# Kernel optimization log

Measured on AMD Instinct MI355X. Metric: run time of the kernel, lower is better.

The kernel has to match this reference:

```python
import jax, jax.numpy as jnp
import numpy as np

D_IN = 1024
D_OUT = 1024


def setup_inputs() -> dict:
    key = jax.random.key(0)
    kx, kq, kk, kv = jax.random.split(key, 4)
    B, S = 4, 2048
    scale = 1.0 / np.sqrt(D_IN)
    return {
        "x": jax.random.normal(kx, (B, S, D_IN), dtype=jnp.float32),
        "Wq": jax.random.normal(kq, (D_IN, D_OUT), dtype=jnp.float32) * scale,
        "Wk": jax.random.normal(kk, (D_IN, D_OUT), dtype=jnp.float32) * scale,
        "Wv": jax.random.normal(kv, (D_IN, D_OUT), dtype=jnp.float32) * scale,
    }


def reference(x, Wq, Wk, Wv):
    # x: [B, S, D_in]; single-head causal attention (dropout=0 -> identity)
    q = jnp.einsum("bsd,de->bse", x, Wq)
    k = jnp.einsum("bsd,de->bse", x, Wk)
    v = jnp.einsum("bsd,de->bse", x, Wv)
    S = x.shape[1]
    d_k = k.shape[-1]
    scores = jnp.einsum("bqe,bke->bqk", q, k) / jnp.sqrt(jnp.float32(d_k))
    causal = jnp.tril(jnp.ones((S, S), dtype=bool))  # True = keep
    scores = jnp.where(causal, scores, -jnp.inf)
    weights = jax.nn.softmax(scores, axis=-1)
    return jnp.einsum("bqk,bke->bqe", weights, v)
```

## Files before the change

kernel.cpp:

```cpp
#include <hip/hip_runtime.h>

typedef unsigned short u16;
typedef __bf16 bf16x8_v __attribute__((ext_vector_type(8)));
typedef float f32x4 __attribute__((ext_vector_type(4)));

__device__ __forceinline__ u16 f2bf(float f) {
    unsigned u = __float_as_uint(f);
    unsigned r = u + 0x7fffu + ((u >> 16) & 1u);
    return (u16)(r >> 16);
}
__device__ __forceinline__ float bf2f(u16 h) {
    return __uint_as_float(((unsigned)h) << 16);
}

__device__ __forceinline__ void gll16(const u16* g, u16* l) {
    __builtin_amdgcn_global_load_lds(
        (const __attribute__((address_space(1))) void*)g,
        (__attribute__((address_space(3))) void*)l, 16, 0, 0);
}

#define EXP_SHIFT 12.0f

__global__ __launch_bounds__(256) void k_cvt_x(const float* __restrict__ x,
                                               u16* __restrict__ y, int n) {
    int i = (blockIdx.x * 256 + threadIdx.x) * 8;
    if (i < n) {
        float4 a = *(const float4*)(x + i);
        float4 b = *(const float4*)(x + i + 4);
        union { int4 p; u16 h[8]; } o;
        o.h[0] = f2bf(a.x); o.h[1] = f2bf(a.y); o.h[2] = f2bf(a.z); o.h[3] = f2bf(a.w);
        o.h[4] = f2bf(b.x); o.h[5] = f2bf(b.y); o.h[6] = f2bf(b.z); o.h[7] = f2bf(b.w);
        *(int4*)(y + i) = o.p;
    }
}

__global__ __launch_bounds__(256) void k_cvt_w3(const float* __restrict__ Wq,
                                                const float* __restrict__ Wk,
                                                const float* __restrict__ Wv,
                                                u16* __restrict__ Wt3) {
    __shared__ float tile[32][33];
    const int z = blockIdx.z;
    const float* W = (z == 0) ? Wq : (z == 1) ? Wk : Wv;
    u16* Wt = Wt3 + (size_t)z * 1024 * 1024;
    int bx = blockIdx.x;
    int by = blockIdx.y;
    int tx = threadIdx.x & 31;
    int ty = threadIdx.x >> 5;
#pragma unroll
    for (int r = 0; r < 4; ++r)
        tile[ty + r * 8][tx] = W[(by * 32 + ty + r * 8) * 1024 + bx * 32 + tx];
    __syncthreads();
#pragma unroll
    for (int r = 0; r < 4; ++r)
        Wt[(bx * 32 + ty + r * 8) * 1024 + by * 32 + tx] =
            f2bf(tile[tx][ty + r * 8]);
}

__device__ __forceinline__ void gemm_core_nt(const u16* __restrict__ A,
                                             const u16* __restrict__ B,
                                             int lda, int ldb, int kLen,
                                             u16* smem, f32x4 acc[4][4]) {
    u16* As = smem;
    u16* Bs = smem + 128 * 32;
    const int tid = threadIdx.x;
    const int wave = tid >> 6;
    const int lane = tid & 63;
    const int r0 = tid >> 2, o0 = (tid & 3) * 8;
    const int r1 = r0 + 64;
    u16* AsW0 = As + wave * 512;
    u16* AsW1 = As + 2048 + wave * 512;
    u16* BsW0 = Bs + wave * 512;
    u16* BsW1 = Bs + 2048 + wave * 512;

    const int wm = (wave >> 1) * 64;
    const int wn = (wave & 1) * 64;
    const int row16 = lane & 15;
    const int quad = lane >> 4;

#pragma unroll
    for (int i = 0; i < 4; ++i)
#pragma unroll
        for (int j = 0; j < 4; ++j) {
            f32x4 z = {0.f, 0.f, 0.f, 0.f};
            acc[i][j] = z;
        }

    const u16* Ag0 = A + r0 * lda + o0;
    const u16* Ag1 = A + r1 * lda + o0;
    const u16* Bg0 = B + r0 * ldb + o0;
    const u16* Bg1 = B + r1 * ldb + o0;

    const int ktiles = kLen >> 5;
    for (int kt = 0; kt < ktiles; ++kt) {
        __syncthreads();
        gll16(Ag0 + kt * 32, AsW0);
        gll16(Ag1 + kt * 32, AsW1);
        gll16(Bg0 + kt * 32, BsW0);
        gll16(Bg1 + kt * 32, BsW1);
        __syncthreads();
        bf16x8_v af[4], bfv[4];
#pragma unroll
        for (int i = 0; i < 4; ++i)
            af[i] = *(const bf16x8_v*)(As + (wm + i * 16 + row16) * 32 + quad * 8);
#pragma unroll
        for (int j = 0; j < 4; ++j)
            bfv[j] = *(const bf16x8_v*)(Bs + (wn + j * 16 + row16) * 32 + quad * 8);
#pragma unroll
        for (int i = 0; i < 4; ++i)
#pragma unroll
            for (int j = 0; j < 4; ++j)
                acc[i][j] = __builtin_amdgcn_mfma_f32_16x16x32_bf16(
                    af[i], bfv[j], acc[i][j], 0, 0, 0);
    }
}

__device__ __forceinline__ void epi_bf16(const f32x4 acc[4][4], u16* smem,
                                         u16* __restrict__ g, int ldg) {
    const int tid = threadIdx.x;
    const int wave = tid >> 6, lane = tid & 63;
    const int row16 = lane & 15, quad = lane >> 4;
    u16* Ts = smem + wave * 2048;
#pragma unroll
    for (int jh = 0; jh < 2; ++jh) {
#pragma unroll
        for (int i = 0; i < 4; ++i)
#pragma unroll
            for (int jj = 0; jj < 2; ++jj) {
                const int j = jh * 2 + jj;
#pragma unroll
                for (int r = 0; r < 4; ++r)
                    Ts[(i * 16 + quad * 4 + r) * 32 + jj * 16 + row16] =
                        f2bf(acc[i][j][r]);
            }
#pragma unroll
        for (int s = 0; s < 4; ++s) {
            const int row = s * 16 + (lane >> 2);
            int4 val = *(const int4*)(Ts + row * 32 + (lane & 3) * 8);
            *(int4*)(g + (size_t)row * ldg + jh * 32 + (lane & 3) * 8) = val;
        }
    }
}

__global__ __launch_bounds__(256, 3) void k_gemm_proj(const u16* __restrict__ X,
                                                      const u16* __restrict__ Wt3,
                                                      u16* __restrict__ Qb,
                                                      u16* __restrict__ Kb,
                                                      u16* __restrict__ Vt) {
    __shared__ u16 smem[128 * 64];
    const int n0g = blockIdx.x * 128, m0 = blockIdx.y * 128;
    f32x4 acc[4][4];
    gemm_core_nt(X + (size_t)m0 * 1024, Wt3 + (size_t)n0g * 1024, 1024, 1024, 1024,
                 smem, acc);
    const int tid = threadIdx.x, wave = tid >> 6, lane = tid & 63;
    const int wm = (wave >> 1) * 64, wn = (wave & 1) * 64;
    const int row16 = lane & 15, quad = lane >> 4;
    if (n0g < 2048) {
        u16* Y = (n0g < 1024) ? Qb : Kb;
        const int n0 = n0g & 1023;
        __syncthreads();
        epi_bf16(acc, smem, Y + (size_t)(m0 + wm) * 1024 + n0 + wn, 1024);
    } else {
        const int n0 = n0g - 2048;
#pragma unroll
        for (int i = 0; i < 4; ++i)
#pragma unroll
            for (int j = 0; j < 4; ++j) {
                int m = m0 + wm + i * 16 + quad * 4;
                int n = n0 + wn + j * 16 + row16;
                int b = m >> 11, s = m & 2047;
                union { ushort4 u4; u16 h[4]; } o;
#pragma unroll
                for (int r = 0; r < 4; ++r) o.h[r] = f2bf(acc[i][j][r]);
                *(ushort4*)(Vt + ((size_t)b * 1024 + n) * 2048 + s) = o.u4;
            }
    }
}

__global__ __launch_bounds__(256, 3) void k_gemm_scores(const u16* __restrict__ Q,
                                                        const u16* __restrict__ Kb,
                                                        u16* __restrict__ Sb,
                                                        float* __restrict__ Srow) {
    __shared__ u16 smem[128 * 64];
    int t = blockIdx.x, b = blockIdx.y;
    int mt = 0;
    while ((mt + 1) * (mt + 2) / 2 <= t) ++mt;
    int nt = t - mt * (mt + 1) / 2;
    const u16* Qp = Q + (size_t)b * 2048 * 1024 + (size_t)mt * 128 * 1024;
    const u16* Kp = Kb + (size_t)b * 2048 * 1024 + (size_t)nt * 128 * 1024;
    u16* Sp = Sb + (size_t)b * 2048 * 2048;
    f32x4 acc[4][4];
    gemm_core_nt(Qp, Kp, 1024, 1024, 1024, smem, acc);
    const int tid = threadIdx.x, wave = tid >> 6, lane = tid & 63;
    const int wm = (wave >> 1) * 64, wn = (wave & 1) * 64;
    const int row16 = lane & 15, quad = lane >> 4;
    const int mBase = mt * 128 + wm;
    const int nBase = nt * 128 + wn;
    u16* Ts = smem + wave * 2048;
    float rs[4][4];
#pragma unroll
    for (int i = 0; i < 4; ++i)
#pragma unroll
        for (int r = 0; r < 4; ++r) rs[i][r] = 0.f;

    __syncthreads();
#pragma unroll
    for (int jh = 0; jh < 2; ++jh) {
#pragma unroll
        for (int i = 0; i < 4; ++i)
#pragma unroll
            for (int jj = 0; jj < 2; ++jj) {
                const int j = jh * 2 + jj;
                const int n = nBase + jh * 32 + jj * 16 + row16;
#pragma unroll
                for (int r = 0; r < 4; ++r) {
                    const int m = mBase + i * 16 + quad * 4 + r;
                    float e = 0.f;
                    if (n <= m)
                        e = __expf(acc[i][j][r] * 0.03125f - EXP_SHIFT);
                    rs[i][r] += e;
                    Ts[(i * 16 + quad * 4 + r) * 32 + jj * 16 + row16] = f2bf(e);
                }
            }
#pragma unroll
        for (int s = 0; s < 4; ++s) {
            const int row = s * 16 + (lane >> 2);
            int4 val = *(const int4*)(Ts + row * 32 + (lane & 3) * 8);
            *(int4*)(Sp + (size_t)(mt * 128 + wm + row) * 2048 +
                     nt * 128 + wn + jh * 32 + (lane & 3) * 8) = val;
        }
    }
    float* Sr = Srow + (size_t)b * 2048;
#pragma unroll
    for (int i = 0; i < 4; ++i)
#pragma unroll
        for (int r = 0; r < 4; ++r) {
            float s = rs[i][r];
#pragma unroll
            for (int off = 1; off < 16; off <<= 1) s += __shfl_xor(s, off);
            if (row16 == 0)
                atomicAdd(Sr + mBase + i * 16 + quad * 4 + r, s);
        }
}

__global__ __launch_bounds__(256, 3) void k_gemm_pv(const u16* __restrict__ P,
                                                    const u16* __restrict__ Vt,
                                                    const float* __restrict__ Srow,
                                                    float* __restrict__ O) {
    __shared__ u16 smem[128 * 64];
    const int nt = blockIdx.x, mt = 15 - blockIdx.y, b = blockIdx.z;
    const u16* Pp = P + (size_t)b * 2048 * 2048 + (size_t)mt * 128 * 2048;
    const u16* Vp = Vt + (size_t)b * 1024 * 2048 + (size_t)nt * 128 * 2048;
    f32x4 acc[4][4];
    gemm_core_nt(Pp, Vp, 2048, 2048, (mt + 1) * 128, smem, acc);
    float* Op = O + (size_t)b * 2048 * 1024;
    const float* Sr = Srow + (size_t)b * 2048;
    const int tid = threadIdx.x, wave = tid >> 6, lane = tid & 63;
    const int wm = (wave >> 1) * 64, wn = (wave & 1) * 64;
    const int row16 = lane & 15, quad = lane >> 4;
    float inv[4][4];
#pragma unroll
    for (int i = 0; i < 4; ++i)
#pragma unroll
        for (int r = 0; r < 4; ++r)
            inv[i][r] = 1.0f / Sr[mt * 128 + wm + i * 16 + quad * 4 + r];
#pragma unroll
    for (int i = 0; i < 4; ++i)
#pragma unroll
        for (int j = 0; j < 4; ++j) {
            int m = mt * 128 + wm + i * 16 + quad * 4;
            int n = nt * 128 + wn + j * 16 + row16;
#pragma unroll
            for (int r = 0; r < 4; ++r)
                Op[(size_t)(m + r) * 1024 + n] = acc[i][j][r] * inv[i][r];
        }
}

extern "C" void kernel_launch(void* const* d_in, const int* in_sizes, int n_in,
                              void* d_out, int out_size, void* d_ws, size_t ws_size,
                              hipStream_t stream) {
    const float* x  = (const float*)d_in[0];
    const float* Wq = (const float*)d_in[1];
    const float* Wk = (const float*)d_in[2];
    const float* Wv = (const float*)d_in[3];
    float* out = (float*)d_out;
    char* ws = (char*)d_ws;

    u16* xb  = (u16*)(ws);
    u16* Wt3 = (u16*)(ws + (16u << 20));
    u16* Qb  = (u16*)(ws + (22u << 20));
    u16* Kb  = (u16*)(ws + (38u << 20));
    u16* Vt  = (u16*)(ws + (54u << 20));
    u16* Sb  = (u16*)(ws + (70u << 20));
    float* Srow = (float*)ws;

    k_cvt_x<<<4096, 256, 0, stream>>>(x, xb, 8192 * 1024);
    k_cvt_w3<<<dim3(32, 32, 3), 256, 0, stream>>>(Wq, Wk, Wv, Wt3);

    k_gemm_proj<<<dim3(24, 64), 256, 0, stream>>>(xb, Wt3, Qb, Kb, Vt);

    hipMemsetAsync(Srow, 0, 8192 * sizeof(float), stream);
    k_gemm_scores<<<dim3(136, 4), 256, 0, stream>>>(Qb, Kb, Sb, Srow);
    k_gemm_pv<<<dim3(8, 16, 4), 256, 0, stream>>>(Sb, Vt, Srow, out);
}
```

Before: 247.2 us.

## Double GEMM K-tile to 64 with XOR-swizzled LDS and coalesced V^T epilogue

The shared GEMM core now stages K-tiles of 64 instead of 32 per barrier pair, halving the number of sync rounds and issuing more global-to-LDS loads per iteration. LDS rows are XOR-swizzled on 16-byte chunks to avoid bank conflicts on the wider rows. The V-transpose epilogue in the projection kernel goes through a padded LDS tile and writes 16-byte coalesced rows instead of scattered 8-byte stores. Shared memory per block doubles (and more for the projection kernel), which may reduce occupancy.

```diff
diff --git a/kernel.cpp b/kernel.cpp
--- a/kernel.cpp
+++ b/kernel.cpp
@@ -61,21 +61,17 @@
                                              int lda, int ldb, int kLen,
                                              u16* smem, f32x4 acc[4][4]) {
     u16* As = smem;
-    u16* Bs = smem + 128 * 32;
+    u16* Bs = smem + 128 * 64;
     const int tid = threadIdx.x;
     const int wave = tid >> 6;
     const int lane = tid & 63;
-    const int r0 = tid >> 2, o0 = (tid & 3) * 8;
-    const int r1 = r0 + 64;
-    u16* AsW0 = As + wave * 512;
-    u16* AsW1 = As + 2048 + wave * 512;
-    u16* BsW0 = Bs + wave * 512;
-    u16* BsW1 = Bs + 2048 + wave * 512;
-
+    const int rowA = tid >> 3;
+    const int kcs  = (tid & 7) ^ (rowA & 7);
+    const int row16 = lane & 15;
+    const int quad = lane >> 4;
+    const int sw = row16 & 7;
     const int wm = (wave >> 1) * 64;
     const int wn = (wave & 1) * 64;
-    const int row16 = lane & 15;
-    const int quad = lane >> 4;
 
 #pragma unroll
     for (int i = 0; i < 4; ++i)
@@ -85,32 +81,43 @@
             acc[i][j] = z;
         }
 
-    const u16* Ag0 = A + r0 * lda + o0;
-    const u16* Ag1 = A + r1 * lda + o0;
-    const u16* Bg0 = B + r0 * ldb + o0;
-    const u16* Bg1 = B + r1 * ldb + o0;
-
-    const int ktiles = kLen >> 5;
+    const u16* Ag[4]; const u16* Bg[4];
+    u16 *AsB[4], *BsB[4];
+#pragma unroll
+    for (int u = 0; u < 4; ++u) {
+        Ag[u] = A + (size_t)(u * 32 + rowA) * lda + kcs * 8;
+        Bg[u] = B + (size_t)(u * 32 + rowA) * ldb + kcs * 8;
+        AsB[u] = As + (u * 256 + wave * 64) * 8;
+        BsB[u] = Bs + (u * 256 + wave * 64) * 8;
+    }
+
+    const int ktiles = kLen >> 6;
     for (int kt = 0; kt < ktiles; ++kt) {
         __syncthreads();
-        gll16(Ag0 + kt * 32, AsW0);
-        gll16(Ag1 + kt * 32, AsW1);
-        gll16(Bg0 + kt * 32, BsW0);
-        gll16(Bg1 + kt * 32, BsW1);
+#pragma unroll
+        for (int u = 0; u < 4; ++u) gll16(Ag[u] + kt * 64, AsB[u]);
+#pragma unroll
+        for (int u = 0; u < 4; ++u) gll16(Bg[u] + kt * 64, BsB[u]);
         __syncthreads();
-        bf16x8_v af[4], bfv[4];
-#pragma unroll
-        for (int i = 0; i < 4; ++i)
-            af[i] = *(const bf16x8_v*)(As + (wm + i * 16 + row16) * 32 + quad * 8);
-#pragma unroll
-        for (int j = 0; j < 4; ++j)
-            bfv[j] = *(const bf16x8_v*)(Bs + (wn + j * 16 + row16) * 32 + quad * 8);
-#pragma unroll
-        for (int i = 0; i < 4; ++i)
+#pragma unroll
+        for (int h = 0; h < 2; ++h) {
+            bf16x8_v af[4], bfv[4];
+            const int cp = (h * 4 + quad);
+#pragma unroll
+            for (int i = 0; i < 4; ++i)
+                af[i] = *(const bf16x8_v*)(As + (wm + i * 16 + row16) * 64 +
+                                           (cp ^ sw) * 8);
 #pragma unroll
             for (int j = 0; j < 4; ++j)
-                acc[i][j] = __builtin_amdgcn_mfma_f32_16x16x32_bf16(
-                    af[i], bfv[j], acc[i][j], 0, 0, 0);
+                bfv[j] = *(const bf16x8_v*)(Bs + (wn + j * 16 + row16) * 64 +
+                                            (cp ^ sw) * 8);
+#pragma unroll
+            for (int i = 0; i < 4; ++i)
+#pragma unroll
+                for (int j = 0; j < 4; ++j)
+                    acc[i][j] = __builtin_amdgcn_mfma_f32_16x16x32_bf16(
+                        af[i], bfv[j], acc[i][j], 0, 0, 0);
+        }
     }
 }
 
@@ -141,38 +148,57 @@
     }
 }
 
+__device__ __forceinline__ void epi_vt(const f32x4 acc[4][4], u16* smem,
+                                       u16* __restrict__ Vt, int m0w, int n0w) {
+    const int tid = threadIdx.x;
+    const int wave = tid >> 6, lane = tid & 63;
+    const int row16 = lane & 15, quad = lane >> 4;
+    const int b = m0w >> 11;
+    const int sBase = m0w & 2047;
+    u16* Ts = smem + wave * 4608;
+#pragma unroll
+    for (int p = 0; p < 2; ++p) {
+#pragma unroll
+        for (int i = 0; i < 4; ++i)
+#pragma unroll
+            for (int jj = 0; jj < 2; ++jj) {
+                const int j = p * 2 + jj;
+                union { unsigned long long d; u16 h[4]; } o;
+#pragma unroll
+                for (int r = 0; r < 4; ++r) o.h[r] = f2bf(acc[i][j][r]);
+                *(unsigned long long*)(Ts + (jj * 16 + row16) * 72 +
+                                       i * 16 + quad * 4) = o.d;
+            }
+#pragma unroll
+        for (int rr = 0; rr < 4; ++rr) {
+            const int ln = rr * 8 + (lane >> 3);
+            const int ck = lane & 7;
+            int4 val = *(const int4*)(Ts + ln * 72 + ck * 8);
+            const int n = n0w + p * 32 + ln;
+            *(int4*)(Vt + ((size_t)b * 1024 + n) * 2048 + sBase + ck * 8) = val;
+        }
+    }
+}
+
 __global__ __launch_bounds__(256, 3) void k_gemm_proj(const u16* __restrict__ X,
                                                       const u16* __restrict__ Wt3,
                                                       u16* __restrict__ Qb,
                                                       u16* __restrict__ Kb,
                                                       u16* __restrict__ Vt) {
-    __shared__ u16 smem[128 * 64];
+    __shared__ u16 smem[18432];
     const int n0g = blockIdx.x * 128, m0 = blockIdx.y * 128;
     f32x4 acc[4][4];
     gemm_core_nt(X + (size_t)m0 * 1024, Wt3 + (size_t)n0g * 1024, 1024, 1024, 1024,
                  smem, acc);
-    const int tid = threadIdx.x, wave = tid >> 6, lane = tid & 63;
+    const int tid = threadIdx.x, wave = tid >> 6;
     const int wm = (wave >> 1) * 64, wn = (wave & 1) * 64;
-    const int row16 = lane & 15, quad = lane >> 4;
+    __syncthreads();
     if (n0g < 2048) {
         u16* Y = (n0g < 1024) ? Qb : Kb;
         const int n0 = n0g & 1023;
-        __syncthreads();
         epi_bf16(acc, smem, Y + (size_t)(m0 + wm) * 1024 + n0 + wn, 1024);
     } else {
-        const int n0 = n0g - 2048;
-#pragma unroll
-        for (int i = 0; i < 4; ++i)
-#pragma unroll
-            for (int j = 0; j < 4; ++j) {
-                int m = m0 + wm + i * 16 + quad * 4;
-                int n = n0 + wn + j * 16 + row16;
-                int b = m >> 11, s = m & 2047;
-                union { ushort4 u4; u16 h[4]; } o;
-#pragma unroll
-                for (int r = 0; r < 4; ++r) o.h[r] = f2bf(acc[i][j][r]);
-                *(ushort4*)(Vt + ((size_t)b * 1024 + n) * 2048 + s) = o.u4;
-            }
+        epi_vt(acc, smem, Vt, m0 + wm, (n0g - 2048) + wn);
     }
 }
 
@@ -180,7 +206,7 @@
                                                         const u16* __restrict__ Kb,
                                                         u16* __restrict__ Sb,
                                                         float* __restrict__ Srow) {
-    __shared__ u16 smem[128 * 64];
+    __shared__ u16 smem[16384];
     int t = blockIdx.x, b = blockIdx.y;
     int mt = 0;
     while ((mt + 1) * (mt + 2) / 2 <= t) ++mt;
@@ -225,8 +251,8 @@
         for (int s = 0; s < 4; ++s) {
             const int row = s * 16 + (lane >> 2);
             int4 val = *(const int4*)(Ts + row * 32 + (lane & 3) * 8);
-            *(int4*)(Sp + (size_t)(mt * 128 + wm + row) * 2048 +
-                     nt * 128 + wn + jh * 32 + (lane & 3) * 8) = val;
+            *(int4*)(Sp + (size_t)(mBase + row) * 2048 +
+                     nBase + jh * 32 + (lane & 3) * 8) = val;
         }
     }
     float* Sr = Srow + (size_t)b * 2048;
@@ -246,7 +272,7 @@
                                                     const u16* __restrict__ Vt,
                                                     const float* __restrict__ Srow,
                                                     float* __restrict__ O) {
-    __shared__ u16 smem[128 * 64];
+    __shared__ u16 smem[16384];
     const int nt = blockIdx.x, mt = 15 - blockIdx.y, b = blockIdx.z;
     const u16* Pp = P + (size_t)b * 2048 * 2048 + (size_t)mt * 128 * 2048;
     const u16* Vp = Vt + (size_t)b * 1024 * 2048 + (size_t)nt * 128 * 2048;
```

Measured after the change: 225.8 us. 8.7% less time.
